# Performance work log

Hardware: AMD Instinct MI355X
Metric: run time of the kernel (lower is better)

Reference implementation:

```python
import jax, jax.numpy as jnp
import numpy as np

N_EDGES = 320000
N_PARTICLES = 10000
EMBED = 256
N_RBF = 16
OUT_EMBED = 512


def setup_inputs() -> dict:
    key = jax.random.key(0)
    ks = jax.random.split(key, 9)
    s = 0.05
    return {
        "messages": jax.random.normal(ks[0], (N_EDGES, EMBED), dtype=jnp.float32),
        "rbf": jax.random.normal(ks[1], (N_EDGES, N_RBF), dtype=jnp.float32),
        "idx_i": jax.random.randint(ks[2], (N_EDGES,), 0, N_PARTICLES, dtype=jnp.int32),
        "W_rbf": jax.random.normal(ks[3], (N_RBF, EMBED), dtype=jnp.float32) * s,
        "W_up": jax.random.normal(ks[4], (EMBED, OUT_EMBED), dtype=jnp.float32) * s,
        "W_d0": jax.random.normal(ks[5], (OUT_EMBED, OUT_EMBED), dtype=jnp.float32) * s,
        "b_d0": jnp.zeros((OUT_EMBED,), dtype=jnp.float32),
        "W_d1": jax.random.normal(ks[6], (OUT_EMBED, OUT_EMBED), dtype=jnp.float32) * s,
        "b_d1": jnp.zeros((OUT_EMBED,), dtype=jnp.float32),
        "W_final": jax.random.normal(ks[7], (OUT_EMBED, 1), dtype=jnp.float32) * s,
    }


def reference(messages, rbf, idx_i, W_rbf, W_up, W_d0, b_d0, W_d1, b_d1, W_final):
    # rbf_dense: [n_edges, n_rbf] @ [n_rbf, embed] -> gate per edge
    transformed_rbf = rbf @ W_rbf
    gated = messages * transformed_rbf                      # [n_edges, embed]
    # high-precision scatter-add over receiver atoms (fp32 accumulation)
    summed = jax.ops.segment_sum(gated, idx_i, num_segments=N_PARTICLES)
    up = summed @ W_up                                      # [n_particles, out_embed]
    up = jax.nn.swish(up @ W_d0 + b_d0)
    up = jax.nn.swish(up @ W_d1 + b_d1)
    per_atom_targets = up @ W_final                         # [n_particles, 1]
    return per_atom_targets
```

## Files before the change

### kernel.cpp

```cpp
#include <hip/hip_runtime.h>
#include <hip/hip_bf16.h>
#include <math.h>

#define N_EDGES_C 320000
#define N_PART 10000
#define EMBED 256
#define NRBF 16
#define OUTE 512

typedef __attribute__((ext_vector_type(8))) short short8;
typedef __attribute__((ext_vector_type(4))) float float4v;

#define WS_SUMMED   0
#define WS_BUF0     6000000
#define WS_BUF1     17000000
#define WS_WTUP     28000000
#define WS_WTD0     28300000
#define WS_WTD1     28900000
#define WS_CNT      29500000
#define WS_CUR      29540000
#define WS_OFF      29580000
#define WS_ELIST    29640000

__global__ __launch_bounds__(256) void hist_kernel(
    const int* __restrict__ idx_i, int* __restrict__ cnt)
{
    int e = blockIdx.x * 256 + threadIdx.x;
    if (e < N_EDGES_C) atomicAdd(&cnt[idx_i[e]], 1);
}

__global__ __launch_bounds__(1024) void scan_kernel(
    const int* __restrict__ cnt, int* __restrict__ off)
{
    __shared__ int s[1024];
    const int t = threadIdx.x;
    const int base = t * 10;
    int v[10];
    int loc = 0;
#pragma unroll
    for (int i = 0; i < 10; ++i) {
        int idx = base + i;
        int c = (idx < N_PART) ? cnt[idx] : 0;
        v[i] = c;
        loc += c;
    }
    s[t] = loc;
    __syncthreads();
    for (int d = 1; d < 1024; d <<= 1) {
        int x = (t >= d) ? s[t - d] : 0;
        __syncthreads();
        s[t] += x;
        __syncthreads();
    }
    int pre = (t > 0) ? s[t - 1] : 0;
#pragma unroll
    for (int i = 0; i < 10; ++i) {
        int idx = base + i;
        if (idx < N_PART) off[idx] = pre;
        pre += v[i];
    }
}

__global__ __launch_bounds__(256) void fill_kernel(
    const int* __restrict__ idx_i, const int* __restrict__ off,
    int* __restrict__ cur, int* __restrict__ elist)
{
    int e = blockIdx.x * 256 + threadIdx.x;
    if (e >= N_EDGES_C) return;
    int p = idx_i[e];
    int pos = atomicAdd(&cur[p], 1);
    elist[off[p] + pos] = e;
}

__global__ __launch_bounds__(256) void gather_kernel(
    const float* __restrict__ messages, const float* __restrict__ rbf,
    const float* __restrict__ W_rbf, const int* __restrict__ off,
    const int* __restrict__ cnt, const int* __restrict__ elist,
    __hip_bfloat16* __restrict__ summed)
{
    __shared__ float red[4][EMBED];
    const int tid  = threadIdx.x;
    const int wave = tid >> 6;
    const int lane = tid & 63;
    const int c4   = lane << 2;
    const int p    = blockIdx.x;

    float4v wr[16];
#pragma unroll
    for (int k = 0; k < 16; ++k)
        wr[k] = *(const float4v*)(W_rbf + k * EMBED + c4);

    const int base = off[p];
    const int deg  = cnt[p];

    float4v acc = {0.f, 0.f, 0.f, 0.f};

    int j = wave;
    int e_next = (j < deg) ? elist[base + j] : 0;
    for (; j < deg; j += 4) {
        const int e = e_next;
        if (j + 4 < deg) e_next = elist[base + j + 4];
        const float4v* r4 = (const float4v*)(rbf + (size_t)e * NRBF);
        const float4v r0 = r4[0], r1 = r4[1], r2 = r4[2], r3 = r4[3];
        const float4v m  = *(const float4v*)(messages + (size_t)e * EMBED + c4);
        float4v t = {0.f, 0.f, 0.f, 0.f};
#define GATE(rv, comp, kk)                                   \
        t[0] = fmaf(rv[comp], wr[kk][0], t[0]);              \
        t[1] = fmaf(rv[comp], wr[kk][1], t[1]);              \
        t[2] = fmaf(rv[comp], wr[kk][2], t[2]);              \
        t[3] = fmaf(rv[comp], wr[kk][3], t[3]);
        GATE(r0, 0, 0)  GATE(r0, 1, 1)  GATE(r0, 2, 2)  GATE(r0, 3, 3)
        GATE(r1, 0, 4)  GATE(r1, 1, 5)  GATE(r1, 2, 6)  GATE(r1, 3, 7)
        GATE(r2, 0, 8)  GATE(r2, 1, 9)  GATE(r2, 2, 10) GATE(r2, 3, 11)
        GATE(r3, 0, 12) GATE(r3, 1, 13) GATE(r3, 2, 14) GATE(r3, 3, 15)
#undef GATE
        acc[0] = fmaf(m[0], t[0], acc[0]);
        acc[1] = fmaf(m[1], t[1], acc[1]);
        acc[2] = fmaf(m[2], t[2], acc[2]);
        acc[3] = fmaf(m[3], t[3], acc[3]);
    }

    *(float4v*)&red[wave][c4] = acc;
    __syncthreads();
    const float s = red[0][tid] + red[1][tid] + red[2][tid] + red[3][tid];
    summed[(size_t)p * EMBED + tid] = __float2bfloat16(s);
}

__global__ __launch_bounds__(256) void transpose_cvt_all(
    const float* __restrict__ W_up, const float* __restrict__ W_d0,
    const float* __restrict__ W_d1, __hip_bfloat16* __restrict__ wt_up,
    __hip_bfloat16* __restrict__ wt_d0, __hip_bfloat16* __restrict__ wt_d1)
{
    const int z = blockIdx.z;
    const float* W = (z == 0) ? W_up : (z == 1) ? W_d0 : W_d1;
    __hip_bfloat16* Wt = (z == 0) ? wt_up : (z == 1) ? wt_d0 : wt_d1;
    const int K = (z == 0) ? EMBED : OUTE;
    const int N = OUTE;
    if (blockIdx.y * 32 >= K) return;

    __shared__ float t[32][33];
    const int bn = blockIdx.x * 32;
    const int bk = blockIdx.y * 32;
    const int x = threadIdx.x & 31;
    const int y8 = threadIdx.x >> 5;
#pragma unroll
    for (int yy = y8; yy < 32; yy += 8)
        t[yy][x] = W[(size_t)(bk + yy) * N + bn + x];
    __syncthreads();
#pragma unroll
    for (int yy = y8; yy < 32; yy += 8)
        Wt[(size_t)(bn + yy) * K + bk + x] = __float2bfloat16(t[x][yy]);
}

#define BM 128
#define BN 128
#define BK 32
#define LDSP 40

template <int ACT, int FUSE>
__global__ __launch_bounds__(256) void gemm_mfma(
    const __hip_bfloat16* __restrict__ A,
    const __hip_bfloat16* __restrict__ Bt,
    const float* __restrict__ bias,
    __hip_bfloat16* __restrict__ C,
    const float* __restrict__ Wf,
    float* __restrict__ out,
    int M, int K, int N)
{
    __shared__ short As[BM * LDSP];
    __shared__ short Bs[BN * LDSP];

    const int tid  = threadIdx.x;
    const int bm   = blockIdx.x * BM;
    const int bn   = blockIdx.y * BN;
    const int wave = tid >> 6;
    const int lane = tid & 63;
    const int wm   = (wave >> 1) * 64;
    const int wn   = (wave & 1) * 64;
    const int l16  = lane & 15;
    const int quad = lane >> 4;

    float4v acc[4][4];
#pragma unroll
    for (int i = 0; i < 4; ++i)
#pragma unroll
        for (int j = 0; j < 4; ++j)
#pragma unroll
            for (int r = 0; r < 4; ++r) acc[i][j][r] = 0.f;

    const int sr = tid >> 1;
    const int sh = (tid & 1) * 16;

    for (int k0 = 0; k0 < K; k0 += BK) {
        short8 av0, av1;
        if (bm + sr < M) {
            const short8* ga = (const short8*)((const short*)A + (size_t)(bm + sr) * K + k0 + sh);
            av0 = ga[0];
            av1 = ga[1];
        } else {
#pragma unroll
            for (int i = 0; i < 8; ++i) { av0[i] = 0; av1[i] = 0; }
        }
        *(short8*)&As[sr * LDSP + sh]     = av0;
        *(short8*)&As[sr * LDSP + sh + 8] = av1;
        const short8* gb = (const short8*)((const short*)Bt + (size_t)(bn + sr) * K + k0 + sh);
        short8 bv0 = gb[0], bv1 = gb[1];
        *(short8*)&Bs[sr * LDSP + sh]     = bv0;
        *(short8*)&Bs[sr * LDSP + sh + 8] = bv1;
        __syncthreads();

        short8 af[4], bf[4];
#pragma unroll
        for (int mt = 0; mt < 4; ++mt)
            af[mt] = *(const short8*)&As[(wm + mt * 16 + l16) * LDSP + quad * 8];
#pragma unroll
        for (int nt = 0; nt < 4; ++nt)
            bf[nt] = *(const short8*)&Bs[(wn + nt * 16 + l16) * LDSP + quad * 8];
#pragma unroll
        for (int mt = 0; mt < 4; ++mt)
#pragma unroll
            for (int nt = 0; nt < 4; ++nt)
                acc[mt][nt] = __builtin_amdgcn_mfma_f32_16x16x32_bf16(
                    af[mt], bf[nt], acc[mt][nt], 0, 0, 0);
        __syncthreads();
    }

    if (!FUSE) {
#pragma unroll
        for (int mt = 0; mt < 4; ++mt) {
            const int row0 = bm + wm + mt * 16 + quad * 4;
#pragma unroll
            for (int nt = 0; nt < 4; ++nt) {
                const int col = bn + wn + nt * 16 + l16;
                const float bv = bias ? bias[col] : 0.f;
#pragma unroll
                for (int r = 0; r < 4; ++r) {
                    const int rr = row0 + r;
                    if (rr < M) {
                        float v = acc[mt][nt][r] + bv;
                        if (ACT == 1) v = v / (1.f + expf(-v));
                        C[(size_t)rr * N + col] = __float2bfloat16(v);
                    }
                }
            }
        }
    } else {
        float bv[4], wfv[4];
#pragma unroll
        for (int nt = 0; nt < 4; ++nt) {
            const int col = bn + wn + nt * 16 + l16;
            bv[nt]  = bias ? bias[col] : 0.f;
            wfv[nt] = Wf[col];
        }
#pragma unroll
        for (int mt = 0; mt < 4; ++mt) {
#pragma unroll
            for (int r = 0; r < 4; ++r) {
                const int row = bm + wm + mt * 16 + quad * 4 + r;
                float s = 0.f;
#pragma unroll
                for (int nt = 0; nt < 4; ++nt) {
                    float v = acc[mt][nt][r] + bv[nt];
                    if (ACT == 1) v = v / (1.f + expf(-v));
                    s = fmaf(v, wfv[nt], s);
                }
#pragma unroll
                for (int o = 8; o > 0; o >>= 1) s += __shfl_down(s, o);
                if (l16 == 0 && row < M) atomicAdd(&out[row], s);
            }
        }
    }
}

extern "C" void kernel_launch(void* const* d_in, const int* in_sizes, int n_in,
                              void* d_out, int out_size, void* d_ws, size_t ws_size,
                              hipStream_t stream) {
    const float* messages = (const float*)d_in[0];
    const float* rbf      = (const float*)d_in[1];
    const int*   idx_i    = (const int*)d_in[2];
    const float* W_rbf    = (const float*)d_in[3];
    const float* W_up     = (const float*)d_in[4];
    const float* W_d0     = (const float*)d_in[5];
    const float* b_d0     = (const float*)d_in[6];
    const float* W_d1     = (const float*)d_in[7];
    const float* b_d1     = (const float*)d_in[8];
    const float* W_final  = (const float*)d_in[9];
    float* out = (float*)d_out;

    char* ws = (char*)d_ws;
    __hip_bfloat16* summed = (__hip_bfloat16*)(ws + WS_SUMMED);
    __hip_bfloat16* buf0   = (__hip_bfloat16*)(ws + WS_BUF0);
    __hip_bfloat16* buf1   = (__hip_bfloat16*)(ws + WS_BUF1);
    __hip_bfloat16* wt_up  = (__hip_bfloat16*)(ws + WS_WTUP);
    __hip_bfloat16* wt_d0  = (__hip_bfloat16*)(ws + WS_WTD0);
    __hip_bfloat16* wt_d1  = (__hip_bfloat16*)(ws + WS_WTD1);
    int* cnt   = (int*)(ws + WS_CNT);
    int* cur   = (int*)(ws + WS_CUR);
    int* offp  = (int*)(ws + WS_OFF);
    int* elist = (int*)(ws + WS_ELIST);

    hipMemsetAsync(ws + WS_CNT, 0, 80000, stream);
    hipMemsetAsync(d_out, 0, (size_t)N_PART * sizeof(float), stream);

    hist_kernel<<<(N_EDGES_C + 255) / 256, 256, 0, stream>>>(idx_i, cnt);
    scan_kernel<<<1, 1024, 0, stream>>>(cnt, offp);
    fill_kernel<<<(N_EDGES_C + 255) / 256, 256, 0, stream>>>(idx_i, offp, cur, elist);

    transpose_cvt_all<<<dim3(OUTE / 32, OUTE / 32, 3), 256, 0, stream>>>(
        W_up, W_d0, W_d1, wt_up, wt_d0, wt_d1);

    gather_kernel<<<N_PART, 256, 0, stream>>>(messages, rbf, W_rbf, offp, cnt,
                                              elist, summed);

    dim3 g((N_PART + BM - 1) / BM, OUTE / BN);
    gemm_mfma<0, 0><<<g, 256, 0, stream>>>(summed, wt_up, nullptr, buf0,
                                           nullptr, nullptr, N_PART, EMBED, OUTE);
    gemm_mfma<1, 0><<<g, 256, 0, stream>>>(buf0, wt_d0, b_d0, buf1,
                                           nullptr, nullptr, N_PART, OUTE, OUTE);
    gemm_mfma<1, 1><<<g, 256, 0, stream>>>(buf1, wt_d1, b_d1, nullptr,
                                           W_final, out, N_PART, OUTE, OUTE);
}
```

Measured before the change: 650.8 us.

## Compute RBF gate with split-bf16 MFMA over edge chunks and atomic segment sums

Replaces the per-particle gather kernel with an edge-chunked kernel. It computes rbf@W_rbf for 32 sorted edges at a time using bf16 MFMA, with a hi/lo split to keep near-fp32 accuracy. The kernel then multiplies by messages and accumulates runs of equal receiver into an fp32 buffer with atomics, and a separate pass converts that buffer to bf16. The aim is to move the gate FMAs onto matrix cores and to balance work evenly across edges instead of across particles with uneven degree. The cost is an extra 10MB memset, atomics at chunk boundaries, extra launches, and a shared-memory round trip for the product.

```diff
diff --git a/kernel.cpp b/kernel.cpp
--- a/kernel.cpp
+++ b/kernel.cpp
@@ -9,7 +9,13 @@
 #define OUTE 512
 
 typedef __attribute__((ext_vector_type(8))) short short8;
+typedef __attribute__((ext_vector_type(4))) short short4v;
 typedef __attribute__((ext_vector_type(4))) float float4v;
+
+__device__ __forceinline__ short bfbits(float x) {
+    __hip_bfloat16 h = __float2bfloat16(x);
+    return *(short*)&h;
+}
 
 #define WS_SUMMED   0
 #define WS_BUF0     6000000
@@ -21,6 +27,8 @@
 #define WS_CUR      29540000
 #define WS_OFF      29580000
 #define WS_ELIST    29640000
+#define WS_WRT      30920000
+#define WS_SUMF     30960000
 
 __global__ __launch_bounds__(256) void hist_kernel(
     const int* __restrict__ idx_i, int* __restrict__ cnt)
@@ -72,58 +80,153 @@
     elist[off[p] + pos] = e;
 }
 
-__global__ __launch_bounds__(256) void gather_kernel(
+__global__ __launch_bounds__(256) void prep_wrbf(
+    const float* __restrict__ W_rbf, __hip_bfloat16* __restrict__ wrt)
+{
+    const int n = threadIdx.x;
+    short row[64];
+#pragma unroll
+    for (int k = 0; k < 16; ++k) {
+        const float w = W_rbf[k * EMBED + n];
+        const short h = bfbits(w);
+        __hip_bfloat16 hb = *(__hip_bfloat16*)&h;
+        const short l = bfbits(w - __bfloat162float(hb));
+        row[k] = h; row[16 + k] = h; row[32 + k] = l; row[48 + k] = 0;
+    }
+    short* dst = (short*)wrt + n * 64;
+#pragma unroll
+    for (int g = 0; g < 8; ++g) {
+        short8 v;
+#pragma unroll
+        for (int i = 0; i < 8; ++i) v[i] = row[g * 8 + i];
+        *(short8*)(dst + g * 8) = v;
+    }
+}
+
+#define CHUNK 32
+#define ASTR 72
+#define PSTR 260
+
+__global__ __launch_bounds__(256) void gather_mfma(
     const float* __restrict__ messages, const float* __restrict__ rbf,
-    const float* __restrict__ W_rbf, const int* __restrict__ off,
-    const int* __restrict__ cnt, const int* __restrict__ elist,
-    __hip_bfloat16* __restrict__ summed)
-{
-    __shared__ float red[4][EMBED];
+    const int* __restrict__ idx_i, const int* __restrict__ elist,
+    const __hip_bfloat16* __restrict__ wrt,
+    float* __restrict__ sumf)
+{
+    __shared__ short A[CHUNK * ASTR];
+    __shared__ float P[CHUNK * PSTR];
+    __shared__ int el[CHUNK];
+    __shared__ int pid[CHUNK];
+
     const int tid  = threadIdx.x;
     const int wave = tid >> 6;
     const int lane = tid & 63;
-    const int c4   = lane << 2;
-    const int p    = blockIdx.x;
-
-    float4v wr[16];
-#pragma unroll
-    for (int k = 0; k < 16; ++k)
-        wr[k] = *(const float4v*)(W_rbf + k * EMBED + c4);
-
-    const int base = off[p];
-    const int deg  = cnt[p];
-
-    float4v acc = {0.f, 0.f, 0.f, 0.f};
-
-    int j = wave;
-    int e_next = (j < deg) ? elist[base + j] : 0;
-    for (; j < deg; j += 4) {
-        const int e = e_next;
-        if (j + 4 < deg) e_next = elist[base + j + 4];
-        const float4v* r4 = (const float4v*)(rbf + (size_t)e * NRBF);
-        const float4v r0 = r4[0], r1 = r4[1], r2 = r4[2], r3 = r4[3];
-        const float4v m  = *(const float4v*)(messages + (size_t)e * EMBED + c4);
-        float4v t = {0.f, 0.f, 0.f, 0.f};
-#define GATE(rv, comp, kk)                                   \
-        t[0] = fmaf(rv[comp], wr[kk][0], t[0]);              \
-        t[1] = fmaf(rv[comp], wr[kk][1], t[1]);              \
-        t[2] = fmaf(rv[comp], wr[kk][2], t[2]);              \
-        t[3] = fmaf(rv[comp], wr[kk][3], t[3]);
-        GATE(r0, 0, 0)  GATE(r0, 1, 1)  GATE(r0, 2, 2)  GATE(r0, 3, 3)
-        GATE(r1, 0, 4)  GATE(r1, 1, 5)  GATE(r1, 2, 6)  GATE(r1, 3, 7)
-        GATE(r2, 0, 8)  GATE(r2, 1, 9)  GATE(r2, 2, 10) GATE(r2, 3, 11)
-        GATE(r3, 0, 12) GATE(r3, 1, 13) GATE(r3, 2, 14) GATE(r3, 3, 15)
-#undef GATE
-        acc[0] = fmaf(m[0], t[0], acc[0]);
-        acc[1] = fmaf(m[1], t[1], acc[1]);
-        acc[2] = fmaf(m[2], t[2], acc[2]);
-        acc[3] = fmaf(m[3], t[3], acc[3]);
-    }
-
-    *(float4v*)&red[wave][c4] = acc;
+    const int l16  = lane & 15;
+    const int quad = lane >> 4;
+    const int base = blockIdx.x * CHUNK;
+
+    short8 bfr[4][2];
+#pragma unroll
+    for (int i = 0; i < 4; ++i) {
+        const int col = (wave * 4 + i) * 16 + l16;
+#pragma unroll
+        for (int s = 0; s < 2; ++s)
+            bfr[i][s] = *(const short8*)((const short*)wrt + col * 64 + s * 32 + quad * 8);
+    }
+
+    if (tid < CHUNK) {
+        const int e = elist[base + tid];
+        el[tid] = e;
+        pid[tid] = idx_i[e];
+    }
     __syncthreads();
-    const float s = red[0][tid] + red[1][tid] + red[2][tid] + red[3][tid];
-    summed[(size_t)p * EMBED + tid] = __float2bfloat16(s);
+
+    if (tid < 128) {
+        const int j  = tid >> 2;
+        const int kq = (tid & 3) << 2;
+        const float4v r = *(const float4v*)(rbf + (size_t)el[j] * NRBF + kq);
+        short4v hi, lo;
+#pragma unroll
+        for (int i = 0; i < 4; ++i) {
+            const short h = bfbits(r[i]);
+            __hip_bfloat16 hb = *(__hip_bfloat16*)&h;
+            hi[i] = h;
+            lo[i] = bfbits(r[i] - __bfloat162float(hb));
+        }
+        *(short4v*)&A[j * ASTR + kq]      = hi;
+        *(short4v*)&A[j * ASTR + 16 + kq] = lo;
+        *(short4v*)&A[j * ASTR + 32 + kq] = hi;
+        *(short4v*)&A[j * ASTR + 48 + kq] = (short4v){0, 0, 0, 0};
+    }
+    __syncthreads();
+
+    float4v acc[2][4];
+#pragma unroll
+    for (int mt = 0; mt < 2; ++mt)
+#pragma unroll
+        for (int i = 0; i < 4; ++i)
+#pragma unroll
+            for (int r = 0; r < 4; ++r) acc[mt][i][r] = 0.f;
+
+    short8 af[2][2];
+#pragma unroll
+    for (int mt = 0; mt < 2; ++mt)
+#pragma unroll
+        for (int s = 0; s < 2; ++s)
+            af[mt][s] = *(const short8*)&A[(mt * 16 + l16) * ASTR + s * 32 + quad * 8];
+#pragma unroll
+    for (int mt = 0; mt < 2; ++mt)
+#pragma unroll
+        for (int i = 0; i < 4; ++i) {
+            acc[mt][i] = __builtin_amdgcn_mfma_f32_16x16x32_bf16(af[mt][0], bfr[i][0], acc[mt][i], 0, 0, 0);
+            acc[mt][i] = __builtin_amdgcn_mfma_f32_16x16x32_bf16(af[mt][1], bfr[i][1], acc[mt][i], 0, 0, 0);
+        }
+#pragma unroll
+    for (int mt = 0; mt < 2; ++mt)
+#pragma unroll
+        for (int i = 0; i < 4; ++i) {
+            const int col  = (wave * 4 + i) * 16 + l16;
+            const int row0 = mt * 16 + quad * 4;
+#pragma unroll
+            for (int r = 0; r < 4; ++r)
+                P[(row0 + r) * PSTR + col] = acc[mt][i][r];
+        }
+    __syncthreads();
+
+    const int c = tid;
+    float a = 0.f;
+    int curp = pid[0];
+#pragma unroll
+    for (int h = 0; h < 2; ++h) {
+        float mv[16];
+#pragma unroll
+        for (int jj = 0; jj < 16; ++jj)
+            mv[jj] = messages[(size_t)el[h * 16 + jj] * EMBED + c];
+#pragma unroll
+        for (int jj = 0; jj < 16; ++jj) {
+            const int j  = h * 16 + jj;
+            const int pj = pid[j];
+            if (pj != curp) {
+                atomicAdd(&sumf[(size_t)curp * EMBED + c], a);
+                a = 0.f;
+                curp = pj;
+            }
+            a = fmaf(mv[jj], P[j * PSTR + c], a);
+        }
+    }
+    atomicAdd(&sumf[(size_t)curp * EMBED + c], a);
+}
+
+__global__ __launch_bounds__(256) void cvt_summed(
+    const float* __restrict__ sf, __hip_bfloat16* __restrict__ sb)
+{
+    const size_t i = ((size_t)blockIdx.x * 256 + threadIdx.x) * 8;
+    const float4v a = *(const float4v*)(sf + i);
+    const float4v b = *(const float4v*)(sf + i + 4);
+    short8 v;
+#pragma unroll
+    for (int r = 0; r < 4; ++r) { v[r] = bfbits(a[r]); v[4 + r] = bfbits(b[r]); }
+    *(short8*)((short*)sb + i) = v;
 }
 
 __global__ __launch_bounds__(256) void transpose_cvt_all(
@@ -294,12 +397,15 @@
     __hip_bfloat16* wt_up  = (__hip_bfloat16*)(ws + WS_WTUP);
     __hip_bfloat16* wt_d0  = (__hip_bfloat16*)(ws + WS_WTD0);
     __hip_bfloat16* wt_d1  = (__hip_bfloat16*)(ws + WS_WTD1);
+    __hip_bfloat16* wrt    = (__hip_bfloat16*)(ws + WS_WRT);
+    float* sumf = (float*)(ws + WS_SUMF);
     int* cnt   = (int*)(ws + WS_CNT);
     int* cur   = (int*)(ws + WS_CUR);
     int* offp  = (int*)(ws + WS_OFF);
     int* elist = (int*)(ws + WS_ELIST);
 
     hipMemsetAsync(ws + WS_CNT, 0, 80000, stream);
+    hipMemsetAsync(ws + WS_SUMF, 0, (size_t)N_PART * EMBED * 4, stream);
     hipMemsetAsync(d_out, 0, (size_t)N_PART * sizeof(float), stream);
 
     hist_kernel<<<(N_EDGES_C + 255) / 256, 256, 0, stream>>>(idx_i, cnt);
@@ -308,9 +414,11 @@
 
     transpose_cvt_all<<<dim3(OUTE / 32, OUTE / 32, 3), 256, 0, stream>>>(
         W_up, W_d0, W_d1, wt_up, wt_d0, wt_d1);
-
-    gather_kernel<<<N_PART, 256, 0, stream>>>(messages, rbf, W_rbf, offp, cnt,
-                                              elist, summed);
+    prep_wrbf<<<1, 256, 0, stream>>>(W_rbf, wrt);
+
+    gather_mfma<<<N_EDGES_C / CHUNK, 256, 0, stream>>>(messages, rbf, idx_i,
+                                                       elist, wrt, sumf);
+    cvt_summed<<<(N_PART * EMBED) / (256 * 8), 256, 0, stream>>>(sumf, summed);
 
     dim3 g((N_PART + BM - 1) / BM, OUTE / BN);
     gemm_mfma<0, 0><<<g, 256, 0, stream>>>(summed, wt_up, nullptr, buf0,
```

New measurement: 628.3 us. 3.5% less time.
